# Kernel optimization log

Measured on AMD Instinct MI355X. Metric: run time of the kernel, lower is better.

## Reference

```python
import jax, jax.numpy as jnp
import numpy as np

HEADS = 8
DIM_HEAD = 64
SCALE = DIM_HEAD ** -0.5


def setup_inputs() -> dict:
    key = jax.random.key(0)
    ks = jax.random.split(key, 8)
    B, Nq, Nk, D = 4, 1024, 2048, 512
    inner = HEADS * DIM_HEAD  # 512
    x = jax.random.normal(ks[0], (B, Nq, D), dtype=jnp.float32)
    context = jax.random.normal(ks[1], (B, Nk, D), dtype=jnp.float32)
    bias = jax.random.normal(ks[2], (B, Nq, Nk), dtype=jnp.float32)
    s = D ** -0.5
    Wq = jax.random.normal(ks[3], (inner, D), dtype=jnp.float32) * s
    Wk = jax.random.normal(ks[4], (inner, D), dtype=jnp.float32) * s
    Wv = jax.random.normal(ks[5], (inner, D), dtype=jnp.float32) * s
    Wo = jax.random.normal(ks[6], (D, inner), dtype=jnp.float32) * s
    bo = jnp.zeros((D,), dtype=jnp.float32)
    return {"x": x, "context": context, "bias": bias,
            "Wq": Wq, "Wk": Wk, "Wv": Wv, "Wo": Wo, "bo": bo}


def reference(x, context, bias, Wq, Wk, Wv, Wo, bo):
    B, Nq, _ = x.shape
    # torch Linear: y = x @ W.T ; reshape (h d) -> b h n d
    q = (x @ Wq.T).reshape(B, Nq, HEADS, DIM_HEAD).transpose(0, 2, 1, 3)
    k = (context @ Wk.T).reshape(B, -1, HEADS, DIM_HEAD).transpose(0, 2, 1, 3)
    v = (context @ Wv.T).reshape(B, -1, HEADS, DIM_HEAD).transpose(0, 2, 1, 3)
    # explicit-score fallback path (bias supplied)
    scores = jnp.einsum('bhqd,bhkd->bhqk', q, k) * SCALE
    scores = scores + bias[:, None, :, :]  # 3D bias -> (B,1,Nq,Nk)
    attn = jax.nn.softmax(scores, axis=-1)
    out = jnp.einsum('bhqk,bhkd->bhqd', attn, v)
    out = out.transpose(0, 2, 1, 3).reshape(B, Nq, HEADS * DIM_HEAD)
    return out @ Wo.T + bo
```

## Files before the change

### kernel.cpp

```cpp
#include <hip/hip_runtime.h>

#define H 8
#define DH 64
#define NQ 1024
#define NK 2048
#define DIN 512
#define B 4
#define KSPLIT 2
#define KRANGE (NK / KSPLIT)
#define KTILES (KRANGE / 64)

typedef __bf16 bf16;
typedef __bf16 bf16x8 __attribute__((ext_vector_type(8)));
typedef __bf16 bf16x4 __attribute__((ext_vector_type(4)));
typedef float floatx4 __attribute__((ext_vector_type(4)));

__device__ inline void gload16(const void* g, void* l) {
  __builtin_amdgcn_global_load_lds(
      (const __attribute__((address_space(1))) void*)g,
      (__attribute__((address_space(3))) void*)l, 16, 0, 0);
}

__global__ void cvt_all(const float* __restrict__ x, const float* __restrict__ ctx,
                        const float* __restrict__ wq, const float* __restrict__ wk,
                        const float* __restrict__ wv, const float* __restrict__ wo,
                        bf16* xb, bf16* cb, bf16* wqb, bf16* wkb, bf16* wvb, bf16* wob) {
  long i = ((long)blockIdx.x * 256 + threadIdx.x) * 4;
  const float* s; bf16* d; long o;
  if (i < 2097152)      { s = x;   d = xb;  o = i; }
  else if (i < 6291456) { s = ctx; d = cb;  o = i - 2097152; }
  else if (i < 6553600) { s = wq;  d = wqb; o = i - 6291456; }
  else if (i < 6815744) { s = wk;  d = wkb; o = i - 6553600; }
  else if (i < 7077888) { s = wv;  d = wvb; o = i - 6815744; }
  else                  { s = wo;  d = wob; o = i - 7077888; }
  float4 f = *(const float4*)(s + o);
  bf16x4 v = { (bf16)f.x, (bf16)f.y, (bf16)f.z, (bf16)f.w };
  *(bf16x4*)(d + o) = v;
}

__global__ __launch_bounds__(256) void gemm_qkv(
    const bf16* __restrict__ xb, const bf16* __restrict__ cb,
    const bf16* __restrict__ wqb, const bf16* __restrict__ wkb, const bf16* __restrict__ wvb,
    bf16* __restrict__ qb, bf16* __restrict__ kb, bf16* __restrict__ vtb) {
  const int which = blockIdx.z;
  if (which == 0 && blockIdx.y >= 32) return;
  const bf16* A = (which == 0) ? xb : cb;
  const bf16* W = (which == 0) ? wqb : ((which == 1) ? wkb : wvb);
  bf16* outb = (which == 0) ? qb : ((which == 1) ? kb : vtb);
  const int logT = (which == 0) ? 10 : 11;
  const float scale = (which == 0) ? 0.125f : 1.0f;
  const bool vmode = (which == 2);

  __shared__ bf16 Al[2][128 * 32];
  __shared__ bf16 Bl[2][128 * 32];
  const int t = threadIdx.x;
  const int lane = t & 63, w = t >> 6;
  const int ln = lane & 15, quad = lane >> 4;
  const int wm = (w >> 1) * 64, wn = (w & 1) * 64;
  const int rowBase = blockIdx.y * 128;
  const int colBase = blockIdx.x * 128;

  floatx4 acc[4][4] = {};
  const int c0 = t, c1 = t + 256;
  const int r0 = c0 >> 2, o0 = (c0 & 3) * 8;
  const int r1 = c1 >> 2, o1 = (c1 & 3) * 8;
  const bf16* Ab = A + (size_t)rowBase * DIN;
  const bf16* Wb = W + (size_t)colBase * DIN;

  gload16(Ab + (size_t)r0 * DIN + o0, &Al[0][c0 * 8]);
  gload16(Ab + (size_t)r1 * DIN + o1, &Al[0][c1 * 8]);
  gload16(Wb + (size_t)r0 * DIN + o0, &Bl[0][c0 * 8]);
  gload16(Wb + (size_t)r1 * DIN + o1, &Bl[0][c1 * 8]);
  __syncthreads();

  for (int k0 = 0; k0 < DIN; k0 += 32) {
    const int cur = (k0 >> 5) & 1, nxt = cur ^ 1;
    if (k0 + 32 < DIN) {
      gload16(Ab + (size_t)r0 * DIN + k0 + 32 + o0, &Al[nxt][c0 * 8]);
      gload16(Ab + (size_t)r1 * DIN + k0 + 32 + o1, &Al[nxt][c1 * 8]);
      gload16(Wb + (size_t)r0 * DIN + k0 + 32 + o0, &Bl[nxt][c0 * 8]);
      gload16(Wb + (size_t)r1 * DIN + k0 + 32 + o1, &Bl[nxt][c1 * 8]);
    }
    bf16x8 af[4], bfr[4];
#pragma unroll
    for (int i = 0; i < 4; i++)
      af[i] = *(const bf16x8*)&Al[cur][(wm + i * 16 + ln) * 32 + quad * 8];
#pragma unroll
    for (int j = 0; j < 4; j++)
      bfr[j] = *(const bf16x8*)&Bl[cur][(wn + j * 16 + ln) * 32 + quad * 8];
#pragma unroll
    for (int i = 0; i < 4; i++)
#pragma unroll
      for (int j = 0; j < 4; j++)
        acc[i][j] = __builtin_amdgcn_mfma_f32_16x16x32_bf16(af[i], bfr[j], acc[i][j], 0, 0, 0);
    __syncthreads();
  }

  const int T = 1 << logT;
#pragma unroll
  for (int i = 0; i < 4; i++)
#pragma unroll
    for (int j = 0; j < 4; j++)
#pragma unroll
      for (int r = 0; r < 4; r++) {
        const int m = rowBase + wm + i * 16 + quad * 4 + r;
        const int n = colBase + wn + j * 16 + ln;
        const float v = acc[i][j][r] * scale;
        const int bb = m >> logT, tok = m & (T - 1);
        const int hh = n >> 6, d = n & 63;
        if (!vmode)
          outb[((((size_t)(bb * H + hh)) << logT) + tok) * DH + d] = (bf16)v;
        else
          outb[(((size_t)(bb * H + hh) * DH + d) << logT) + tok] = (bf16)v;
      }
}

__global__ __launch_bounds__(256) void gemm_out(
    const bf16* __restrict__ A, const bf16* __restrict__ W,
    float* __restrict__ outf, const float* __restrict__ bo) {
  __shared__ bf16 Al[2][128 * 32];
  __shared__ bf16 Bl[2][128 * 32];
  const int t = threadIdx.x;
  const int lane = t & 63, w = t >> 6;
  const int ln = lane & 15, quad = lane >> 4;
  const int wm = (w >> 1) * 64, wn = (w & 1) * 64;
  const int rowBase = blockIdx.y * 128;
  const int colBase = blockIdx.x * 128;

  floatx4 acc[4][4] = {};
  const int c0 = t, c1 = t + 256;
  const int r0 = c0 >> 2, o0 = (c0 & 3) * 8;
  const int r1 = c1 >> 2, o1 = (c1 & 3) * 8;
  const bf16* Ab = A + (size_t)rowBase * DIN;
  const bf16* Wb = W + (size_t)colBase * DIN;

  gload16(Ab + (size_t)r0 * DIN + o0, &Al[0][c0 * 8]);
  gload16(Ab + (size_t)r1 * DIN + o1, &Al[0][c1 * 8]);
  gload16(Wb + (size_t)r0 * DIN + o0, &Bl[0][c0 * 8]);
  gload16(Wb + (size_t)r1 * DIN + o1, &Bl[0][c1 * 8]);
  __syncthreads();

  for (int k0 = 0; k0 < DIN; k0 += 32) {
    const int cur = (k0 >> 5) & 1, nxt = cur ^ 1;
    if (k0 + 32 < DIN) {
      gload16(Ab + (size_t)r0 * DIN + k0 + 32 + o0, &Al[nxt][c0 * 8]);
      gload16(Ab + (size_t)r1 * DIN + k0 + 32 + o1, &Al[nxt][c1 * 8]);
      gload16(Wb + (size_t)r0 * DIN + k0 + 32 + o0, &Bl[nxt][c0 * 8]);
      gload16(Wb + (size_t)r1 * DIN + k0 + 32 + o1, &Bl[nxt][c1 * 8]);
    }
    bf16x8 af[4], bfr[4];
#pragma unroll
    for (int i = 0; i < 4; i++)
      af[i] = *(const bf16x8*)&Al[cur][(wm + i * 16 + ln) * 32 + quad * 8];
#pragma unroll
    for (int j = 0; j < 4; j++)
      bfr[j] = *(const bf16x8*)&Bl[cur][(wn + j * 16 + ln) * 32 + quad * 8];
#pragma unroll
    for (int i = 0; i < 4; i++)
#pragma unroll
      for (int j = 0; j < 4; j++)
        acc[i][j] = __builtin_amdgcn_mfma_f32_16x16x32_bf16(af[i], bfr[j], acc[i][j], 0, 0, 0);
    __syncthreads();
  }

#pragma unroll
  for (int i = 0; i < 4; i++)
#pragma unroll
    for (int j = 0; j < 4; j++)
#pragma unroll
      for (int r = 0; r < 4; r++) {
        const int m = rowBase + wm + i * 16 + quad * 4 + r;
        const int n = colBase + wn + j * 16 + ln;
        outf[(size_t)m * DIN + n] = acc[i][j][r] + bo[n];
      }
}

__global__ __launch_bounds__(256) void attn_fwd(
    const bf16* __restrict__ q, const bf16* __restrict__ k,
    const bf16* __restrict__ vt, const float* __restrict__ bias,
    float* __restrict__ op0, float* __restrict__ op1, float* __restrict__ lpart) {
  __shared__ bf16 KL[2][64 * 64];
  __shared__ bf16 VL[2][64 * 64];
  __shared__ bf16 Pl[4][16 * 64];
  const int tid = threadIdx.x;
  const int lane = tid & 63, w = tid >> 6;
  const int ln = lane & 15, quad = lane >> 4;
  const int hh = blockIdx.y;
  const int b = blockIdx.z >> 1, ks = blockIdx.z & 1;
  const int q0 = blockIdx.x * 64;
  const int k0 = ks * KRANGE;
  const size_t bh = (size_t)b * H + hh;
  const bf16* qp = q + bh * NQ * DH;
  const bf16* kp = k + bh * NK * DH;
  const bf16* vp = vt + bh * DH * NK;
  const float* bp = bias + ((size_t)b * NQ + q0 + w * 16 + quad * 4) * NK + ln;
  bf16* pl = &Pl[w][0];

  const int si0 = tid, si1 = tid + 256;
  const int sr0 = si0 >> 3, sc0 = (si0 & 7) ^ (sr0 & 7);
  const int sr1 = si1 >> 3, sc1 = (si1 & 7) ^ (sr1 & 7);

  bf16x8 qf[2];
#pragma unroll
  for (int kc = 0; kc < 2; kc++)
    qf[kc] = *(const bf16x8*)(qp + (size_t)(q0 + w * 16 + ln) * DH + kc * 32 + quad * 8);

  floatx4 o[4] = {};
  float lacc[4] = {0.f, 0.f, 0.f, 0.f};
  float bc[4][4], bn[4][4];
  constexpr float L2E = 1.44269504f;
  constexpr float OFF = 34.6246810f;

  gload16(kp + (size_t)(k0 + sr0) * DH + sc0 * 8, &KL[0][si0 * 8]);
  gload16(kp + (size_t)(k0 + sr1) * DH + sc1 * 8, &KL[0][si1 * 8]);
  gload16(vp + (size_t)sr0 * NK + k0 + sc0 * 8, &VL[0][si0 * 8]);
  gload16(vp + (size_t)sr1 * NK + k0 + sc1 * 8, &VL[0][si1 * 8]);
#pragma unroll
  for (int j = 0; j < 4; j++)
#pragma unroll
    for (int r = 0; r < 4; r++)
      bc[j][r] = bp[(size_t)r * NK + k0 + j * 16];
  __syncthreads();

  for (int tt = 0; tt < KTILES; tt++) {
    const int cur = tt & 1, nxt = cur ^ 1;
    if (tt + 1 < KTILES) {
      const int nk1 = k0 + (tt + 1) * 64;
      gload16(kp + (size_t)(nk1 + sr0) * DH + sc0 * 8, &KL[nxt][si0 * 8]);
      gload16(kp + (size_t)(nk1 + sr1) * DH + sc1 * 8, &KL[nxt][si1 * 8]);
      gload16(vp + (size_t)sr0 * NK + nk1 + sc0 * 8, &VL[nxt][si0 * 8]);
      gload16(vp + (size_t)sr1 * NK + nk1 + sc1 * 8, &VL[nxt][si1 * 8]);
#pragma unroll
      for (int j = 0; j < 4; j++)
#pragma unroll
        for (int r = 0; r < 4; r++)
          bn[j][r] = bp[(size_t)r * NK + nk1 + j * 16];
    }

    floatx4 s4[4];
#pragma unroll
    for (int j = 0; j < 4; j++) {
      s4[j][0] = bc[j][0]; s4[j][1] = bc[j][1];
      s4[j][2] = bc[j][2]; s4[j][3] = bc[j][3];
    }
#pragma unroll
    for (int j = 0; j < 4; j++)
#pragma unroll
      for (int kc = 0; kc < 2; kc++) {
        const int kr = j * 16 + ln;
        bf16x8 kf = *(const bf16x8*)&KL[cur][kr * 64 + (((kc * 4 + quad) ^ (kr & 7)) * 8)];
        s4[j] = __builtin_amdgcn_mfma_f32_16x16x32_bf16(qf[kc], kf, s4[j], 0, 0, 0);
      }

#pragma unroll
    for (int j = 0; j < 4; j++)
#pragma unroll
      for (int r = 0; r < 4; r++) {
        const float p = exp2f(fmaf(s4[j][r], L2E, -OFF));
        lacc[r] += p;
        s4[j][r] = p;
      }

#pragma unroll
    for (int j = 0; j < 4; j++)
#pragma unroll
      for (int r = 0; r < 4; r++) {
        const int m = quad * 4 + r;
        pl[m * 64 + (((j * 2 + (ln >> 3)) ^ (m & 7)) * 8) + (ln & 7)] = (bf16)s4[j][r];
      }
    asm volatile("s_waitcnt lgkmcnt(0)" ::: "memory");
    bf16x8 pf[2];
#pragma unroll
    for (int kc = 0; kc < 2; kc++)
      pf[kc] = *(const bf16x8*)&pl[ln * 64 + (((kc * 4 + quad) ^ (ln & 7)) * 8)];
#pragma unroll
    for (int jn = 0; jn < 4; jn++)
#pragma unroll
      for (int kc = 0; kc < 2; kc++) {
        const int vr = jn * 16 + ln;
        bf16x8 vf = *(const bf16x8*)&VL[cur][vr * 64 + (((kc * 4 + quad) ^ (vr & 7)) * 8)];
        o[jn] = __builtin_amdgcn_mfma_f32_16x16x32_bf16(pf[kc], vf, o[jn], 0, 0, 0);
      }

    __syncthreads();
#pragma unroll
    for (int j = 0; j < 4; j++)
#pragma unroll
      for (int r = 0; r < 4; r++)
        bc[j][r] = bn[j][r];
  }

#pragma unroll
  for (int d = 1; d < 16; d <<= 1)
#pragma unroll
    for (int r = 0; r < 4; r++)
      lacc[r] += __shfl_xor(lacc[r], d, 64);

  float* op = (ks ? op1 : op0) +
              ((size_t)b * NQ + q0 + w * 16 + quad * 4) * DIN + hh * 64 + ln;
#pragma unroll
  for (int jn = 0; jn < 4; jn++)
#pragma unroll
    for (int r = 0; r < 4; r++)
      op[(size_t)r * DIN + jn * 16] = o[jn][r];

  if (ln == 0) {
    float4 lv = {lacc[0], lacc[1], lacc[2], lacc[3]};
    *(float4*)&lpart[((size_t)ks * B * H + b * H + hh) * NQ + q0 + w * 16 + quad * 4] = lv;
  }
}

__global__ void combine_kernel(const float* __restrict__ op0, const float* __restrict__ op1,
                               const float* __restrict__ lp, bf16* __restrict__ ab) {
  const int i = blockIdx.x * 256 + threadIdx.x;
  const int idx = i * 4;
  const int row = idx >> 9, col = idx & 511;
  const int b = row >> 10, qq = row & 1023, hh = col >> 6;
  const float4 o0 = *(const float4*)(op0 + idx);
  const float4 o1 = *(const float4*)(op1 + idx);
  const float l = lp[(b * H + hh) * NQ + qq] + lp[B * H * NQ + (b * H + hh) * NQ + qq];
  const float inv = 1.0f / l;
  bf16x4 r = { (bf16)((o0.x + o1.x) * inv), (bf16)((o0.y + o1.y) * inv),
               (bf16)((o0.z + o1.z) * inv), (bf16)((o0.w + o1.w) * inv) };
  *(bf16x4*)(ab + idx) = r;
}

extern "C" void kernel_launch(void* const* d_in, const int* in_sizes, int n_in,
                              void* d_out, int out_size, void* d_ws, size_t ws_size,
                              hipStream_t stream) {
  const float* x    = (const float*)d_in[0];
  const float* ctx  = (const float*)d_in[1];
  const float* bias = (const float*)d_in[2];
  const float* Wq   = (const float*)d_in[3];
  const float* Wk   = (const float*)d_in[4];
  const float* Wv   = (const float*)d_in[5];
  const float* Wo   = (const float*)d_in[6];
  const float* bo   = (const float*)d_in[7];
  float* out = (float*)d_out;

  char* p = (char*)d_ws;
  bf16* xb   = (bf16*)(p + 0);
  bf16* cb   = (bf16*)(p + 4194304);
  bf16* wqb  = (bf16*)(p + 12582912);
  bf16* wkb  = (bf16*)(p + 13107200);
  bf16* wvb  = (bf16*)(p + 13631488);
  bf16* wob  = (bf16*)(p + 14155776);
  bf16* qb   = (bf16*)(p + 14680064);
  bf16* kb   = (bf16*)(p + 18874368);
  bf16* vtb  = (bf16*)(p + 27262976);
  bf16* ab   = (bf16*)(p + 35651584);
  float* op1 = (float*)(p + 39845888);
  float* lpart = (float*)(p + 48234496);
  float* op0 = (float*)cb;

  cvt_all<<<7168, 256, 0, stream>>>(x, ctx, Wq, Wk, Wv, Wo, xb, cb, wqb, wkb, wvb, wob);
  gemm_qkv<<<dim3(4, 64, 3), 256, 0, stream>>>(xb, cb, wqb, wkb, wvb, qb, kb, vtb);
  attn_fwd<<<dim3(NQ / 64, H, B * KSPLIT), 256, 0, stream>>>(qb, kb, vtb, bias, op0, op1, lpart);
  combine_kernel<<<2048, 256, 0, stream>>>(op0, op1, lpart, ab);
  gemm_out<<<dim3(4, 32), 256, 0, stream>>>(ab, wob, out, bo);
}
```

Before: 199.7 us.

## Fuse split-K combine into output GEMM and shrink attention blocks to two waves

Drops the separate combine kernel. The output projection GEMM now reads both fp32 partial outputs, normalises them by the summed row sums, converts to bf16 and stages the result into LDS itself, which removes a launch and a bf16 round trip. The attention kernel moves to 128-thread blocks covering 32 query rows with single-buffered K/V tiles, so there are more, smaller blocks but no prefetch overlap. Row sums are now computed with an MFMA against a ones vector instead of per-lane adds and shuffles. The fused GEMM A-load becomes synchronous register loads, which could stall its pipeline.

```diff
diff --git a/kernel.cpp b/kernel.cpp
--- a/kernel.cpp
+++ b/kernel.cpp
@@ -9,6 +9,7 @@
 #define KSPLIT 2
 #define KRANGE (NK / KSPLIT)
 #define KTILES (KRANGE / 64)
+#define BHNQ (B * H * NQ)
 
 typedef __bf16 bf16;
 typedef __bf16 bf16x8 __attribute__((ext_vector_type(8)));
@@ -115,8 +116,122 @@
       }
 }
 
+__global__ __launch_bounds__(128) void attn_fwd(
+    const bf16* __restrict__ q, const bf16* __restrict__ k,
+    const bf16* __restrict__ vt, const float* __restrict__ bias,
+    float* __restrict__ op0, float* __restrict__ op1, float* __restrict__ lpart) {
+  __shared__ bf16 KL[64 * 64];
+  __shared__ bf16 VL[64 * 64];
+  __shared__ bf16 Pl[2][16 * 64];
+  const int tid = threadIdx.x;
+  const int lane = tid & 63, w = tid >> 6;
+  const int ln = lane & 15, quad = lane >> 4;
+  const int hh = blockIdx.y;
+  const int b = blockIdx.z >> 1, ks = blockIdx.z & 1;
+  const int q0 = blockIdx.x * 32;
+  const int k0 = ks * KRANGE;
+  const size_t bh = (size_t)b * H + hh;
+  const bf16* qp = q + bh * NQ * DH;
+  const bf16* kp = k + bh * NK * DH;
+  const bf16* vp = vt + bh * DH * NK;
+  const float* bp = bias + ((size_t)b * NQ + q0 + w * 16 + quad * 4) * NK + ln;
+  bf16* pl = &Pl[w][0];
+
+  bf16x8 qf[2];
+#pragma unroll
+  for (int kc = 0; kc < 2; kc++)
+    qf[kc] = *(const bf16x8*)(qp + (size_t)(q0 + w * 16 + ln) * DH + kc * 32 + quad * 8);
+
+  floatx4 o[4] = {};
+  floatx4 lac = {};
+  const bf16x8 ones = {(bf16)1.f, (bf16)1.f, (bf16)1.f, (bf16)1.f,
+                       (bf16)1.f, (bf16)1.f, (bf16)1.f, (bf16)1.f};
+  constexpr float L2E = 1.44269504f;
+  constexpr float OFF = 34.6246810f;
+
+  for (int tt = 0; tt < KTILES; tt++) {
+    const int nk0 = k0 + tt * 64;
+#pragma unroll
+    for (int s = 0; s < 4; s++) {
+      const int i = s * 128 + tid;
+      const int sr = i >> 3, sc = (i & 7) ^ (sr & 7);
+      gload16(kp + (size_t)(nk0 + sr) * DH + sc * 8, &KL[i * 8]);
+      gload16(vp + (size_t)sr * NK + nk0 + sc * 8, &VL[i * 8]);
+    }
+    float bc[4][4];
+#pragma unroll
+    for (int j = 0; j < 4; j++)
+#pragma unroll
+      for (int r = 0; r < 4; r++)
+        bc[j][r] = bp[(size_t)r * NK + nk0 + j * 16];
+    __syncthreads();
+
+    floatx4 s4[4];
+#pragma unroll
+    for (int j = 0; j < 4; j++) {
+      s4[j][0] = bc[j][0]; s4[j][1] = bc[j][1];
+      s4[j][2] = bc[j][2]; s4[j][3] = bc[j][3];
+    }
+#pragma unroll
+    for (int j = 0; j < 4; j++)
+#pragma unroll
+      for (int kc = 0; kc < 2; kc++) {
+        const int kr = j * 16 + ln;
+        bf16x8 kf = *(const bf16x8*)&KL[kr * 64 + (((kc * 4 + quad) ^ (kr & 7)) * 8)];
+        s4[j] = __builtin_amdgcn_mfma_f32_16x16x32_bf16(qf[kc], kf, s4[j], 0, 0, 0);
+      }
+
+#pragma unroll
+    for (int j = 0; j < 4; j++)
+#pragma unroll
+      for (int r = 0; r < 4; r++)
+        s4[j][r] = exp2f(fmaf(s4[j][r], L2E, -OFF));
+
+#pragma unroll
+    for (int j = 0; j < 4; j++)
+#pragma unroll
+      for (int r = 0; r < 4; r++) {
+        const int m = quad * 4 + r;
+        pl[m * 64 + (((j * 2 + (ln >> 3)) ^ (m & 7)) * 8) + (ln & 7)] = (bf16)s4[j][r];
+      }
+    asm volatile("s_waitcnt lgkmcnt(0)" ::: "memory");
+    bf16x8 pf[2];
+#pragma unroll
+    for (int kc = 0; kc < 2; kc++)
+      pf[kc] = *(const bf16x8*)&pl[ln * 64 + (((kc * 4 + quad) ^ (ln & 7)) * 8)];
+
+#pragma unroll
+    for (int kc = 0; kc < 2; kc++)
+      lac = __builtin_amdgcn_mfma_f32_16x16x32_bf16(pf[kc], ones, lac, 0, 0, 0);
+
+#pragma unroll
+    for (int jn = 0; jn < 4; jn++)
+#pragma unroll
+      for (int kc = 0; kc < 2; kc++) {
+        const int vr = jn * 16 + ln;
+        bf16x8 vf = *(const bf16x8*)&VL[vr * 64 + (((kc * 4 + quad) ^ (vr & 7)) * 8)];
+        o[jn] = __builtin_amdgcn_mfma_f32_16x16x32_bf16(pf[kc], vf, o[jn], 0, 0, 0);
+      }
+    __syncthreads();
+  }
+
+  float* op = (ks ? op1 : op0) +
+              ((size_t)b * NQ + q0 + w * 16 + quad * 4) * DIN + hh * 64 + ln;
+#pragma unroll
+  for (int jn = 0; jn < 4; jn++)
+#pragma unroll
+    for (int r = 0; r < 4; r++)
+      op[(size_t)r * DIN + jn * 16] = o[jn][r];
+
+  if (ln == 0) {
+    float4 lv = {lac[0], lac[1], lac[2], lac[3]};
+    *(float4*)&lpart[((size_t)ks * B * H + b * H + hh) * NQ + q0 + w * 16 + quad * 4] = lv;
+  }
+}
+
 __global__ __launch_bounds__(256) void gemm_out(
-    const bf16* __restrict__ A, const bf16* __restrict__ W,
+    const float* __restrict__ op0, const float* __restrict__ op1,
+    const float* __restrict__ lp, const bf16* __restrict__ W,
     float* __restrict__ outf, const float* __restrict__ bo) {
   __shared__ bf16 Al[2][128 * 32];
   __shared__ bf16 Bl[2][128 * 32];
@@ -131,22 +246,54 @@
   const int c0 = t, c1 = t + 256;
   const int r0 = c0 >> 2, o0 = (c0 & 3) * 8;
   const int r1 = c1 >> 2, o1 = (c1 & 3) * 8;
-  const bf16* Ab = A + (size_t)rowBase * DIN;
+  const int m0 = rowBase + r0, m1 = rowBase + r1;
   const bf16* Wb = W + (size_t)colBase * DIN;
 
-  gload16(Ab + (size_t)r0 * DIN + o0, &Al[0][c0 * 8]);
-  gload16(Ab + (size_t)r1 * DIN + o1, &Al[0][c1 * 8]);
+  float linv0[8], linv1[8];
+#pragma unroll
+  for (int h = 0; h < 8; h++) {
+    const int i0 = ((m0 >> 10) * H + h) * NQ + (m0 & 1023);
+    const int i1 = ((m1 >> 10) * H + h) * NQ + (m1 & 1023);
+    linv0[h] = 1.0f / (lp[i0] + lp[BHNQ + i0]);
+    linv1[h] = 1.0f / (lp[i1] + lp[BHNQ + i1]);
+  }
+
+#define STAGE_A(K0V, BUF)                                                      \
+  {                                                                            \
+    const float sA = linv0[(K0V) >> 6], sB = linv1[(K0V) >> 6];                \
+    const float* pa0 = op0 + (size_t)m0 * DIN + (K0V) + o0;                    \
+    const float* pa1 = op1 + (size_t)m0 * DIN + (K0V) + o0;                    \
+    const float* pb0 = op0 + (size_t)m1 * DIN + (K0V) + o1;                    \
+    const float* pb1 = op1 + (size_t)m1 * DIN + (K0V) + o1;                    \
+    float4 xa = *(const float4*)pa0, xb2 = *(const float4*)(pa0 + 4);          \
+    float4 ya = *(const float4*)pa1, yb = *(const float4*)(pa1 + 4);           \
+    float4 za = *(const float4*)pb0, zb = *(const float4*)(pb0 + 4);           \
+    float4 ua = *(const float4*)pb1, ub = *(const float4*)(pb1 + 4);           \
+    bf16x8 v0 = {(bf16)((xa.x + ya.x) * sA), (bf16)((xa.y + ya.y) * sA),       \
+                 (bf16)((xa.z + ya.z) * sA), (bf16)((xa.w + ya.w) * sA),       \
+                 (bf16)((xb2.x + yb.x) * sA), (bf16)((xb2.y + yb.y) * sA),     \
+                 (bf16)((xb2.z + yb.z) * sA), (bf16)((xb2.w + yb.w) * sA)};    \
+    bf16x8 v1 = {(bf16)((za.x + ua.x) * sB), (bf16)((za.y + ua.y) * sB),       \
+                 (bf16)((za.z + ua.z) * sB), (bf16)((za.w + ua.w) * sB),       \
+                 (bf16)((zb.x + ub.x) * sB), (bf16)((zb.y + ub.y) * sB),       \
+                 (bf16)((zb.z + ub.z) * sB), (bf16)((zb.w + ub.w) * sB)};      \
+    *(bf16x8*)&Al[BUF][c0 * 8] = v0;                                           \
+    *(bf16x8*)&Al[BUF][c1 * 8] = v1;                                           \
+  }
+
+  STAGE_A(0, 0);
   gload16(Wb + (size_t)r0 * DIN + o0, &Bl[0][c0 * 8]);
   gload16(Wb + (size_t)r1 * DIN + o1, &Bl[0][c1 * 8]);
   __syncthreads();
 
-  for (int k0 = 0; k0 < DIN; k0 += 32) {
-    const int cur = (k0 >> 5) & 1, nxt = cur ^ 1;
-    if (k0 + 32 < DIN) {
-      gload16(Ab + (size_t)r0 * DIN + k0 + 32 + o0, &Al[nxt][c0 * 8]);
-      gload16(Ab + (size_t)r1 * DIN + k0 + 32 + o1, &Al[nxt][c1 * 8]);
-      gload16(Wb + (size_t)r0 * DIN + k0 + 32 + o0, &Bl[nxt][c0 * 8]);
-      gload16(Wb + (size_t)r1 * DIN + k0 + 32 + o1, &Bl[nxt][c1 * 8]);
+#pragma unroll
+  for (int kk = 0; kk < 16; kk++) {
+    const int cur = kk & 1, nxt = cur ^ 1;
+    if (kk < 15) {
+      const int k1 = (kk + 1) * 32;
+      STAGE_A(k1, nxt);
+      gload16(Wb + (size_t)r0 * DIN + k1 + o0, &Bl[nxt][c0 * 8]);
+      gload16(Wb + (size_t)r1 * DIN + k1 + o1, &Bl[nxt][c1 * 8]);
     }
     bf16x8 af[4], bfr[4];
 #pragma unroll
@@ -162,6 +309,7 @@
         acc[i][j] = __builtin_amdgcn_mfma_f32_16x16x32_bf16(af[i], bfr[j], acc[i][j], 0, 0, 0);
     __syncthreads();
   }
+#undef STAGE_A
 
 #pragma unroll
   for (int i = 0; i < 4; i++)
@@ -173,156 +321,6 @@
         const int n = colBase + wn + j * 16 + ln;
         outf[(size_t)m * DIN + n] = acc[i][j][r] + bo[n];
       }
-}
-
-__global__ __launch_bounds__(256) void attn_fwd(
-    const bf16* __restrict__ q, const bf16* __restrict__ k,
-    const bf16* __restrict__ vt, const float* __restrict__ bias,
-    float* __restrict__ op0, float* __restrict__ op1, float* __restrict__ lpart) {
-  __shared__ bf16 KL[2][64 * 64];
-  __shared__ bf16 VL[2][64 * 64];
-  __shared__ bf16 Pl[4][16 * 64];
-  const int tid = threadIdx.x;
-  const int lane = tid & 63, w = tid >> 6;
-  const int ln = lane & 15, quad = lane >> 4;
-  const int hh = blockIdx.y;
-  const int b = blockIdx.z >> 1, ks = blockIdx.z & 1;
-  const int q0 = blockIdx.x * 64;
-  const int k0 = ks * KRANGE;
-  const size_t bh = (size_t)b * H + hh;
-  const bf16* qp = q + bh * NQ * DH;
-  const bf16* kp = k + bh * NK * DH;
-  const bf16* vp = vt + bh * DH * NK;
-  const float* bp = bias + ((size_t)b * NQ + q0 + w * 16 + quad * 4) * NK + ln;
-  bf16* pl = &Pl[w][0];
-
-  const int si0 = tid, si1 = tid + 256;
-  const int sr0 = si0 >> 3, sc0 = (si0 & 7) ^ (sr0 & 7);
-  const int sr1 = si1 >> 3, sc1 = (si1 & 7) ^ (sr1 & 7);
-
-  bf16x8 qf[2];
-#pragma unroll
-  for (int kc = 0; kc < 2; kc++)
-    qf[kc] = *(const bf16x8*)(qp + (size_t)(q0 + w * 16 + ln) * DH + kc * 32 + quad * 8);
-
-  floatx4 o[4] = {};
-  float lacc[4] = {0.f, 0.f, 0.f, 0.f};
-  float bc[4][4], bn[4][4];
-  constexpr float L2E = 1.44269504f;
-  constexpr float OFF = 34.6246810f;
-
-  gload16(kp + (size_t)(k0 + sr0) * DH + sc0 * 8, &KL[0][si0 * 8]);
-  gload16(kp + (size_t)(k0 + sr1) * DH + sc1 * 8, &KL[0][si1 * 8]);
-  gload16(vp + (size_t)sr0 * NK + k0 + sc0 * 8, &VL[0][si0 * 8]);
-  gload16(vp + (size_t)sr1 * NK + k0 + sc1 * 8, &VL[0][si1 * 8]);
-#pragma unroll
-  for (int j = 0; j < 4; j++)
-#pragma unroll
-    for (int r = 0; r < 4; r++)
-      bc[j][r] = bp[(size_t)r * NK + k0 + j * 16];
-  __syncthreads();
-
-  for (int tt = 0; tt < KTILES; tt++) {
-    const int cur = tt & 1, nxt = cur ^ 1;
-    if (tt + 1 < KTILES) {
-      const int nk1 = k0 + (tt + 1) * 64;
-      gload16(kp + (size_t)(nk1 + sr0) * DH + sc0 * 8, &KL[nxt][si0 * 8]);
-      gload16(kp + (size_t)(nk1 + sr1) * DH + sc1 * 8, &KL[nxt][si1 * 8]);
-      gload16(vp + (size_t)sr0 * NK + nk1 + sc0 * 8, &VL[nxt][si0 * 8]);
-      gload16(vp + (size_t)sr1 * NK + nk1 + sc1 * 8, &VL[nxt][si1 * 8]);
-#pragma unroll
-      for (int j = 0; j < 4; j++)
-#pragma unroll
-        for (int r = 0; r < 4; r++)
-          bn[j][r] = bp[(size_t)r * NK + nk1 + j * 16];
-    }
-
-    floatx4 s4[4];
-#pragma unroll
-    for (int j = 0; j < 4; j++) {
-      s4[j][0] = bc[j][0]; s4[j][1] = bc[j][1];
-      s4[j][2] = bc[j][2]; s4[j][3] = bc[j][3];
-    }
-#pragma unroll
-    for (int j = 0; j < 4; j++)
-#pragma unroll
-      for (int kc = 0; kc < 2; kc++) {
-        const int kr = j * 16 + ln;
-        bf16x8 kf = *(const bf16x8*)&KL[cur][kr * 64 + (((kc * 4 + quad) ^ (kr & 7)) * 8)];
-        s4[j] = __builtin_amdgcn_mfma_f32_16x16x32_bf16(qf[kc], kf, s4[j], 0, 0, 0);
-      }
-
-#pragma unroll
-    for (int j = 0; j < 4; j++)
-#pragma unroll
-      for (int r = 0; r < 4; r++) {
-        const float p = exp2f(fmaf(s4[j][r], L2E, -OFF));
-        lacc[r] += p;
-        s4[j][r] = p;
-      }
-
-#pragma unroll
-    for (int j = 0; j < 4; j++)
-#pragma unroll
-      for (int r = 0; r < 4; r++) {
-        const int m = quad * 4 + r;
-        pl[m * 64 + (((j * 2 + (ln >> 3)) ^ (m & 7)) * 8) + (ln & 7)] = (bf16)s4[j][r];
-      }
-    asm volatile("s_waitcnt lgkmcnt(0)" ::: "memory");
-    bf16x8 pf[2];
-#pragma unroll
-    for (int kc = 0; kc < 2; kc++)
-      pf[kc] = *(const bf16x8*)&pl[ln * 64 + (((kc * 4 + quad) ^ (ln & 7)) * 8)];
-#pragma unroll
-    for (int jn = 0; jn < 4; jn++)
-#pragma unroll
-      for (int kc = 0; kc < 2; kc++) {
-        const int vr = jn * 16 + ln;
-        bf16x8 vf = *(const bf16x8*)&VL[cur][vr * 64 + (((kc * 4 + quad) ^ (vr & 7)) * 8)];
-        o[jn] = __builtin_amdgcn_mfma_f32_16x16x32_bf16(pf[kc], vf, o[jn], 0, 0, 0);
-      }
-
-    __syncthreads();
-#pragma unroll
-    for (int j = 0; j < 4; j++)
-#pragma unroll
-      for (int r = 0; r < 4; r++)
-        bc[j][r] = bn[j][r];
-  }
-
-#pragma unroll
-  for (int d = 1; d < 16; d <<= 1)
-#pragma unroll
-    for (int r = 0; r < 4; r++)
-      lacc[r] += __shfl_xor(lacc[r], d, 64);
-
-  float* op = (ks ? op1 : op0) +
-              ((size_t)b * NQ + q0 + w * 16 + quad * 4) * DIN + hh * 64 + ln;
-#pragma unroll
-  for (int jn = 0; jn < 4; jn++)
-#pragma unroll
-    for (int r = 0; r < 4; r++)
-      op[(size_t)r * DIN + jn * 16] = o[jn][r];
-
-  if (ln == 0) {
-    float4 lv = {lacc[0], lacc[1], lacc[2], lacc[3]};
-    *(float4*)&lpart[((size_t)ks * B * H + b * H + hh) * NQ + q0 + w * 16 + quad * 4] = lv;
-  }
-}
-
-__global__ void combine_kernel(const float* __restrict__ op0, const float* __restrict__ op1,
-                               const float* __restrict__ lp, bf16* __restrict__ ab) {
-  const int i = blockIdx.x * 256 + threadIdx.x;
-  const int idx = i * 4;
-  const int row = idx >> 9, col = idx & 511;
-  const int b = row >> 10, qq = row & 1023, hh = col >> 6;
-  const float4 o0 = *(const float4*)(op0 + idx);
-  const float4 o1 = *(const float4*)(op1 + idx);
-  const float l = lp[(b * H + hh) * NQ + qq] + lp[B * H * NQ + (b * H + hh) * NQ + qq];
-  const float inv = 1.0f / l;
-  bf16x4 r = { (bf16)((o0.x + o1.x) * inv), (bf16)((o0.y + o1.y) * inv),
-               (bf16)((o0.z + o1.z) * inv), (bf16)((o0.w + o1.w) * inv) };
-  *(bf16x4*)(ab + idx) = r;
 }
 
 extern "C" void kernel_launch(void* const* d_in, const int* in_sizes, int n_in,
@@ -348,14 +346,12 @@
   bf16* qb   = (bf16*)(p + 14680064);
   bf16* kb   = (bf16*)(p + 18874368);
   bf16* vtb  = (bf16*)(p + 27262976);
-  bf16* ab   = (bf16*)(p + 35651584);
-  float* op1 = (float*)(p + 39845888);
-  float* lpart = (float*)(p + 48234496);
+  float* op1 = (float*)(p + 35651584);
+  float* lpart = (float*)(p + 44040192);
   float* op0 = (float*)cb;
 
   cvt_all<<<7168, 256, 0, stream>>>(x, ctx, Wq, Wk, Wv, Wo, xb, cb, wqb, wkb, wvb, wob);
   gemm_qkv<<<dim3(4, 64, 3), 256, 0, stream>>>(xb, cb, wqb, wkb, wvb, qb, kb, vtb);
-  attn_fwd<<<dim3(NQ / 64, H, B * KSPLIT), 256, 0, stream>>>(qb, kb, vtb, bias, op0, op1, lpart);
-  combine_kernel<<<2048, 256, 0, stream>>>(op0, op1, lpart, ab);
-  gemm_out<<<dim3(4, 32), 256, 0, stream>>>(ab, wob, out, bo);
-}
+  attn_fwd<<<dim3(NQ / 32, H, B * KSPLIT), 128, 0, stream>>>(qb, kb, vtb, bias, op0, op1, lpart);
+  gemm_out<<<dim3(4, 32), 256, 0, stream>>>(op0, op1, lpart, wob, out, bo);
+}
```

Result: slower. 211.2 us (+5.8%).
